# Performance work log

Measured on AMD Instinct MI355X. Metric: run time of the kernel, lower is better.

The kernel has to match this reference:

```python
import jax, jax.numpy as jnp
import numpy as np
from jax.scipy.special import logsumexp

T, N, C, L = 2048, 256, 128, 200
S = 2 * L + 1  # padded label length (blanks interleaved)
NEG = -1e30    # finite -inf surrogate (safe for logsumexp grads)


def setup_inputs() -> dict:
    key = jax.random.key(0)
    k1, k2 = jax.random.split(key)
    # module consumes pred as log-probabilities (adds scores in log space)
    pred = jax.nn.log_softmax(jax.random.normal(k1, (T, N, C), dtype=jnp.float32), axis=-1)
    target = jax.random.randint(k2, (N * L,), 1, C)  # labels in [1, C-1], 0 is blank
    input_length = jnp.full((N,), T, dtype=jnp.int32)
    target_length = jnp.full((N,), L, dtype=jnp.int32)
    return {"pred": pred, "target": target, "input_length": input_length, "target_length": target_length}


def _ctc_loss(pred, target, target_length):
    # Faithful to the original's slicing: start_i = target_length[i-1] for i>0 else 0
    starts = jnp.concatenate([jnp.zeros((1,), jnp.int32), target_length[:-1].astype(jnp.int32)])
    idx = starts[:, None] + jnp.arange(L)[None, :]                     # (N, L)
    labels = target[idx]                                               # (N, L)
    # padded target: blank(0) at even positions, labels at odd positions
    ext = jnp.zeros((N, S), dtype=target.dtype).at[:, 1::2].set(labels)
    pos = jnp.arange(S)
    prev2 = jnp.pad(ext, ((0, 0), (2, 0)))[:, :S]
    # skip transition s-2 -> s allowed iff s is a non-blank position and label differs from s-2
    skip_ok = (pos % 2 == 1)[None, :] & (pos >= 2)[None, :] & (ext != prev2)  # (N, S)

    emit0 = jnp.take_along_axis(pred[0], ext, axis=1)                  # (N, S)
    alpha0 = jnp.full((N, S), NEG, jnp.float32).at[:, 0].set(emit0[:, 0]).at[:, 1].set(emit0[:, 1])

    def step(alpha, pred_t):
        sc = jnp.take_along_axis(pred_t, ext, axis=1)                  # (N, S) emission log-probs
        a1 = jnp.concatenate([jnp.full((N, 1), NEG, alpha.dtype), alpha[:, :-1]], axis=1)
        a2 = jnp.concatenate([jnp.full((N, 2), NEG, alpha.dtype), alpha[:, :-2]], axis=1)
        a2 = jnp.where(skip_ok, a2, NEG)
        new = logsumexp(jnp.stack([alpha, a1, a2], axis=0), axis=0) + sc
        return new, None

    alphaT, _ = jax.lax.scan(step, alpha0, pred[1:])
    # per-sample loss: -logsumexp(alpha[T-1, S-2], alpha[T-1, S-1])
    loss = -logsumexp(alphaT[:, S - 2:], axis=1)                        # (N,)
    return jnp.sum(loss)  # reduction='sum'


def reference(pred, target, input_length, target_length):
    return _ctc_loss(pred, target, target_length)
```

## Files before the change

kernel.cpp:

```cpp
#include <hip/hip_runtime.h>


#define TT 2048
#define NN 256
#define CC 128
#define LL 200

#define K_LOG2E 1.4426950408889634f
#define K_LN2   0.6931471805599453f
#define NEGB   (-1.44e30f)
#define PEN    (-2.0e30f)
#define NC4    131072u

__device__ __forceinline__ float max3f(float a, float b, float c) {
    float r; asm("v_max3_f32 %0, %1, %2, %3" : "=v"(r) : "v"(a), "v"(b), "v"(c)); return r;
}

__global__ __launch_bounds__(256, 1)
void ctc_alpha(const float* __restrict__ pred,
               const int* __restrict__ target,
               const int* __restrict__ tlen,
               float* __restrict__ loss_ws)
{
    __shared__ float blk[5][128][16];
    __shared__ int   flags[8];

    const int tid  = threadIdx.x;
    const int wid  = tid >> 6;
    const int lane = tid & 63;
    const int n    = blockIdx.x;

    if (tid < 8) flags[tid] = (tid >= 4) ? 0x7fffffff : 0;
    for (int i = tid; i < 128 * 16; i += 256) ((float*)blk[4])[i] = PEN;

    const int start = (n == 0) ? 0 : tlen[n - 1];
    const int idx   = (wid << 6) | lane;
    int lab1 = 0; float msk1 = 0.0f;
    if (idx < LL) {
        lab1 = target[start + idx];
        if (idx >= 1 && lab1 != target[start + idx - 1]) msk1 = 1.0f;
    }

    float al0, al1;
    {
        const float eB = pred[n * CC];
        const float eL = pred[n * CC + lab1];
        al0 = (idx == 0) ? K_LOG2E * eB : NEGB;
        al1 = (idx == 0) ? K_LOG2E * eL : NEGB;
    }
    __syncthreads();

    const char* pcRow = (const char*)pred + (size_t)(NN * CC + n * CC) * 4u;
    uint32_t vB = 0u;
    uint32_t vL = (uint32_t)lab1 * 4u;
    asm volatile("" : "+v"(vB), "+v"(vL));
    float scB[16], scL[16];
#pragma unroll
    for (int ph = 0; ph < 16; ++ph) {
        scB[ph] = *(const float*)(pcRow + vB);
        scL[ph] = *(const float*)(pcRow + vL);
        pcRow += NC4;
    }

    float (* const blkC)[16] = blk[(wid == 0) ? 4 : (wid - 1)];
    float (* const blkW)[16] = blk[wid];
    volatile int* pflag = &flags[(wid == 0) ? 7 : (wid - 1)];
    volatile int* mflag = &flags[wid];
    int fval = *pflag;

    float bndA[16], bndB[16], bw[16];
    float bprev = (wid == 0) ? PEN : NEGB;

#define LOAD_BLK(DST, B)                                                       \
    {                                                                          \
        const float4* q = (const float4*)&blkC[B][0];                          \
        const float4 v0 = q[0], v1 = q[1], v2 = q[2], v3 = q[3];               \
        DST[0]=v0.x;  DST[1]=v0.y;  DST[2]=v0.z;  DST[3]=v0.w;                 \
        DST[4]=v1.x;  DST[5]=v1.y;  DST[6]=v1.z;  DST[7]=v1.w;                 \
        DST[8]=v2.x;  DST[9]=v2.y;  DST[10]=v2.z; DST[11]=v2.w;                \
        DST[12]=v3.x; DST[13]=v3.y; DST[14]=v3.z; DST[15]=v3.w;                \
    }

#define STORE_BLK(B)                                                           \
    if (lane == 63) {                                                          \
        float4* d = (float4*)&blkW[B][0];                                      \
        d[0] = make_float4(bw[0],  bw[1],  bw[2],  bw[3]);                     \
        d[1] = make_float4(bw[4],  bw[5],  bw[6],  bw[7]);                     \
        d[2] = make_float4(bw[8],  bw[9],  bw[10], bw[11]);                    \
        d[3] = make_float4(bw[12], bw[13], bw[14], bw[15]);                    \
    }

#define CTC_STEP(PH, BV, PREF)                                                 \
    {                                                                          \
        const float hold = ((PH) == 0) ? bprev : BV[((PH) + 15) & 15];         \
        const int h1i = __builtin_amdgcn_update_dpp(                           \
            __float_as_int(hold), __float_as_int(al1), 0x138, 0xf, 0xf, false);\
        const float h1 = __int_as_float(h1i);                                  \
        const float M  = max3f(al1, al0, h1);                                  \
        const float b1 = fmaf(K_LOG2E, scL[PH], M);                            \
        const float b0 = fmaf(K_LOG2E, scB[PH], M);                            \
        const float e1 = __builtin_amdgcn_exp2f(al1 - M);                      \
        const float e0 = __builtin_amdgcn_exp2f(al0 - M);                      \
        const float eh = __builtin_amdgcn_exp2f(h1 - M);                       \
        const float s1 = fmaf(eh, msk1, e1 + e0);                              \
        const float s0 = e0 + eh;                                              \
        al1 = b1 + __builtin_amdgcn_logf(s1);                                  \
        al0 = b0 + __builtin_amdgcn_logf(s0);                                  \
        bw[PH] = al1;                                                          \
        if (PREF) {                                                            \
            scB[PH] = *(const float*)(pcRow + vB);                             \
            scL[PH] = *(const float*)(pcRow + vL);                             \
            pcRow += NC4;                                                      \
        }                                                                      \
    }

#define RUN_BLOCK(B, BUSE, BPRE, NEED, LASTPREF)                               \
    {                                                                          \
        const int need_ = (NEED);                                              \
        if (fval < need_) { do { fval = *pflag; } while (fval < need_); }      \
        asm volatile("" ::: "memory");                                         \
        LOAD_BLK(BPRE, (B) + 1)                                                \
        CTC_STEP( 0, BUSE, 1) CTC_STEP( 1, BUSE, 1) CTC_STEP( 2, BUSE, 1)      \
        CTC_STEP( 3, BUSE, 1) CTC_STEP( 4, BUSE, 1) CTC_STEP( 5, BUSE, 1)      \
        CTC_STEP( 6, BUSE, 1) CTC_STEP( 7, BUSE, 1) CTC_STEP( 8, BUSE, 1)      \
        CTC_STEP( 9, BUSE, 1) CTC_STEP(10, BUSE, 1) CTC_STEP(11, BUSE, 1)      \
        CTC_STEP(12, BUSE, 1) CTC_STEP(13, BUSE, 1) CTC_STEP(14, BUSE, 1)      \
        CTC_STEP(15, BUSE, LASTPREF)                                           \
        STORE_BLK(B)                                                           \
        asm volatile("" ::: "memory");             \
        if (lane == 0) *mflag = (B) + 1;                                       \
        bprev = BUSE[15];                                                      \
        fval = *pflag;                                                         \
    }

    if (fval < 1) { do { fval = *pflag; } while (fval < 1); }
    asm volatile("" ::: "memory");
    LOAD_BLK(bndA, 0)

    for (int bb = 0; bb < 63; ++bb) {
        RUN_BLOCK(2 * bb,     bndA, bndB, 2 * bb + 2, 1)
        RUN_BLOCK(2 * bb + 1, bndB, bndA, 2 * bb + 3, 1)
    }

    RUN_BLOCK(126, bndA, bndB, 128, 0)

    {
        asm volatile("" ::: "memory");
        CTC_STEP( 0, bndB, 0) CTC_STEP( 1, bndB, 0) CTC_STEP( 2, bndB, 0)
        CTC_STEP( 3, bndB, 0) CTC_STEP( 4, bndB, 0) CTC_STEP( 5, bndB, 0)
        CTC_STEP( 6, bndB, 0) CTC_STEP( 7, bndB, 0) CTC_STEP( 8, bndB, 0)
        CTC_STEP( 9, bndB, 0) CTC_STEP(10, bndB, 0) CTC_STEP(11, bndB, 0)
        CTC_STEP(12, bndB, 0) CTC_STEP(13, bndB, 0) CTC_STEP(14, bndB, 0)
        STORE_BLK(127)
        asm volatile("" ::: "memory");
        if (lane == 0) *mflag = 128;
    }
#undef CTC_STEP
#undef RUN_BLOCK
#undef LOAD_BLK
#undef STORE_BLK

    const float A = __shfl(al1, 7, 64);
    const float B = __shfl(al0, 8, 64);
    if (wid == 3 && lane == 0) {
        const float m  = fmaxf(A, B);
        const float ls = m + __builtin_amdgcn_logf(
            __builtin_amdgcn_exp2f(A - m) + __builtin_amdgcn_exp2f(B - m));
        loss_ws[n] = -ls * K_LN2;
    }
}

__global__ void ctc_reduce(const float* __restrict__ ws, float* __restrict__ out)
{
    const int tid = threadIdx.x;
    float v = ws[tid];
    v += __shfl_down(v, 32);
    v += __shfl_down(v, 16);
    v += __shfl_down(v, 8);
    v += __shfl_down(v, 4);
    v += __shfl_down(v, 2);
    v += __shfl_down(v, 1);
    __shared__ float p[4];
    if ((tid & 63) == 0) p[tid >> 6] = v;
    __syncthreads();
    if (tid == 0) out[0] = (p[0] + p[1]) + (p[2] + p[3]);
}

extern "C" void kernel_launch(void* const* d_in, const int* in_sizes, int n_in,
                              void* d_out, int out_size, void* d_ws, size_t ws_size,
                              hipStream_t stream)
{
    const float* pred   = (const float*)d_in[0];
    const int*   target = (const int*)d_in[1];
    const int*   tlen   = (const int*)d_in[3];
    float* ws = (float*)d_ws;

    ctc_alpha<<<NN, 256, 0, stream>>>(pred, target, tlen, ws);
    ctc_reduce<<<1, NN, 0, stream>>>(ws, (float*)d_out);
}
```

Baseline: 151.0 us.

## Represent CTC alpha as mantissa-exponent pairs instead of log-space values

Replaces the log-space recurrence (max3, three exp2 and two log per step) with a scaled linear-domain form: each alpha is stored as a float mantissa plus an integer exponent. Terms are aligned with ldexp to the maximum exponent and multiplied by exp2 of the emission, and the values are renormalised every four steps. The aim is to drop the transcendental log on the serial dependency chain, but it doubles the DPP shuffles, doubles LDS boundary traffic and register use, and adds integer and ldexp work. It also relies on the mantissas not underflowing between renormalisations.

```diff
diff --git a/kernel.cpp b/kernel.cpp
--- a/kernel.cpp
+++ b/kernel.cpp
@@ -8,13 +8,8 @@
 
 #define K_LOG2E 1.4426950408889634f
 #define K_LN2   0.6931471805599453f
-#define NEGB   (-1.44e30f)
-#define PEN    (-2.0e30f)
-#define NC4    131072u
-
-__device__ __forceinline__ float max3f(float a, float b, float c) {
-    float r; asm("v_max3_f32 %0, %1, %2, %3" : "=v"(r) : "v"(a), "v"(b), "v"(c)); return r;
-}
+#define EDEAD   (-(1 << 28))
+#define NC4     131072u
 
 __global__ __launch_bounds__(256, 1)
 void ctc_alpha(const float* __restrict__ pred,
@@ -22,7 +17,8 @@
                const int* __restrict__ tlen,
                float* __restrict__ loss_ws)
 {
-    __shared__ float blk[5][128][16];
+    __shared__ float blkM[5][128][16];
+    __shared__ int   blkE[5][128][16];
     __shared__ int   flags[8];
 
     const int tid  = threadIdx.x;
@@ -31,7 +27,10 @@
     const int n    = blockIdx.x;
 
     if (tid < 8) flags[tid] = (tid >= 4) ? 0x7fffffff : 0;
-    for (int i = tid; i < 128 * 16; i += 256) ((float*)blk[4])[i] = PEN;
+    for (int i = tid; i < 128 * 16; i += 256) {
+        ((float*)blkM[4])[i] = 0.0f;
+        ((int*)blkE[4])[i]   = EDEAD;
+    }
 
     const int start = (n == 0) ? 0 : tlen[n - 1];
     const int idx   = (wid << 6) | lane;
@@ -41,12 +40,15 @@
         if (idx >= 1 && lab1 != target[start + idx - 1]) msk1 = 1.0f;
     }
 
-    float al0, al1;
+    float m0, m1; int E0, E1;
     {
-        const float eB = pred[n * CC];
-        const float eL = pred[n * CC + lab1];
-        al0 = (idx == 0) ? K_LOG2E * eB : NEGB;
-        al1 = (idx == 0) ? K_LOG2E * eL : NEGB;
+        const float xB = K_LOG2E * pred[n * CC];
+        const float xL = K_LOG2E * pred[n * CC + lab1];
+        const float fB = floorf(xB), fL = floorf(xL);
+        m0 = (idx == 0) ? __builtin_amdgcn_exp2f(xB - fB) : 0.0f;
+        m1 = (idx == 0) ? __builtin_amdgcn_exp2f(xL - fL) : 0.0f;
+        E0 = (idx == 0) ? (int)fB : EDEAD;
+        E1 = (idx == 0) ? (int)fL : EDEAD;
     }
     __syncthreads();
 
@@ -62,51 +64,75 @@
         pcRow += NC4;
     }
 
-    float (* const blkC)[16] = blk[(wid == 0) ? 4 : (wid - 1)];
-    float (* const blkW)[16] = blk[wid];
+    float (* const blkCM)[16] = blkM[(wid == 0) ? 4 : (wid - 1)];
+    int   (* const blkCE)[16] = blkE[(wid == 0) ? 4 : (wid - 1)];
+    float (* const blkWM)[16] = blkM[wid];
+    int   (* const blkWE)[16] = blkE[wid];
     volatile int* pflag = &flags[(wid == 0) ? 7 : (wid - 1)];
     volatile int* mflag = &flags[wid];
     int fval = *pflag;
 
-    float bndA[16], bndB[16], bw[16];
-    float bprev = (wid == 0) ? PEN : NEGB;
-
-#define LOAD_BLK(DST, B)                                                       \
+    float bndAM[16], bndBM[16], bwM[16];
+    int   bndAE[16], bndBE[16], bwE[16];
+    float bprevM = 0.0f;
+    int   bprevE = EDEAD;
+
+#define LOAD_BLK(DM, DE, B)                                                    \
     {                                                                          \
-        const float4* q = (const float4*)&blkC[B][0];                          \
-        const float4 v0 = q[0], v1 = q[1], v2 = q[2], v3 = q[3];               \
-        DST[0]=v0.x;  DST[1]=v0.y;  DST[2]=v0.z;  DST[3]=v0.w;                 \
-        DST[4]=v1.x;  DST[5]=v1.y;  DST[6]=v1.z;  DST[7]=v1.w;                 \
-        DST[8]=v2.x;  DST[9]=v2.y;  DST[10]=v2.z; DST[11]=v2.w;                \
-        DST[12]=v3.x; DST[13]=v3.y; DST[14]=v3.z; DST[15]=v3.w;                \
+        const float4* qm = (const float4*)&blkCM[B][0];                        \
+        const int4*   qe = (const int4*)&blkCE[B][0];                          \
+        const float4 a0 = qm[0], a1 = qm[1], a2 = qm[2], a3 = qm[3];           \
+        const int4   b0 = qe[0], b1 = qe[1], b2 = qe[2], b3 = qe[3];           \
+        DM[0]=a0.x;  DM[1]=a0.y;  DM[2]=a0.z;  DM[3]=a0.w;                     \
+        DM[4]=a1.x;  DM[5]=a1.y;  DM[6]=a1.z;  DM[7]=a1.w;                     \
+        DM[8]=a2.x;  DM[9]=a2.y;  DM[10]=a2.z; DM[11]=a2.w;                    \
+        DM[12]=a3.x; DM[13]=a3.y; DM[14]=a3.z; DM[15]=a3.w;                    \
+        DE[0]=b0.x;  DE[1]=b0.y;  DE[2]=b0.z;  DE[3]=b0.w;                     \
+        DE[4]=b1.x;  DE[5]=b1.y;  DE[6]=b1.z;  DE[7]=b1.w;                     \
+        DE[8]=b2.x;  DE[9]=b2.y;  DE[10]=b2.z; DE[11]=b2.w;                    \
+        DE[12]=b3.x; DE[13]=b3.y; DE[14]=b3.z; DE[15]=b3.w;                    \
     }
 
 #define STORE_BLK(B)                                                           \
     if (lane == 63) {                                                          \
-        float4* d = (float4*)&blkW[B][0];                                      \
-        d[0] = make_float4(bw[0],  bw[1],  bw[2],  bw[3]);                     \
-        d[1] = make_float4(bw[4],  bw[5],  bw[6],  bw[7]);                     \
-        d[2] = make_float4(bw[8],  bw[9],  bw[10], bw[11]);                    \
-        d[3] = make_float4(bw[12], bw[13], bw[14], bw[15]);                    \
-    }
-
-#define CTC_STEP(PH, BV, PREF)                                                 \
+        float4* dm = (float4*)&blkWM[B][0];                                    \
+        int4*   de = (int4*)&blkWE[B][0];                                      \
+        dm[0] = make_float4(bwM[0],  bwM[1],  bwM[2],  bwM[3]);                \
+        dm[1] = make_float4(bwM[4],  bwM[5],  bwM[6],  bwM[7]);                \
+        dm[2] = make_float4(bwM[8],  bwM[9],  bwM[10], bwM[11]);               \
+        dm[3] = make_float4(bwM[12], bwM[13], bwM[14], bwM[15]);               \
+        de[0] = make_int4(bwE[0],  bwE[1],  bwE[2],  bwE[3]);                  \
+        de[1] = make_int4(bwE[4],  bwE[5],  bwE[6],  bwE[7]);                  \
+        de[2] = make_int4(bwE[8],  bwE[9],  bwE[10], bwE[11]);                 \
+        de[3] = make_int4(bwE[12], bwE[13], bwE[14], bwE[15]);                 \
+    }
+
+#define CTC_STEP(PH, BVM, BVE, PREF)                                           \
     {                                                                          \
-        const float hold = ((PH) == 0) ? bprev : BV[((PH) + 15) & 15];         \
-        const int h1i = __builtin_amdgcn_update_dpp(                           \
-            __float_as_int(hold), __float_as_int(al1), 0x138, 0xf, 0xf, false);\
-        const float h1 = __int_as_float(h1i);                                  \
-        const float M  = max3f(al1, al0, h1);                                  \
-        const float b1 = fmaf(K_LOG2E, scL[PH], M);                            \
-        const float b0 = fmaf(K_LOG2E, scB[PH], M);                            \
-        const float e1 = __builtin_amdgcn_exp2f(al1 - M);                      \
-        const float e0 = __builtin_amdgcn_exp2f(al0 - M);                      \
-        const float eh = __builtin_amdgcn_exp2f(h1 - M);                       \
-        const float s1 = fmaf(eh, msk1, e1 + e0);                              \
-        const float s0 = e0 + eh;                                              \
-        al1 = b1 + __builtin_amdgcn_logf(s1);                                  \
-        al0 = b0 + __builtin_amdgcn_logf(s0);                                  \
-        bw[PH] = al1;                                                          \
+        const float holdM = ((PH) == 0) ? bprevM : BVM[((PH) + 15) & 15];      \
+        const int   holdE = ((PH) == 0) ? bprevE : BVE[((PH) + 15) & 15];      \
+        const int mhi = __builtin_amdgcn_update_dpp(                           \
+            __float_as_int(holdM), __float_as_int(m1), 0x138, 0xf, 0xf, false);\
+        const int Eh  = __builtin_amdgcn_update_dpp(                           \
+            holdE, E1, 0x138, 0xf, 0xf, false);                                \
+        const float mh = __int_as_float(mhi);                                  \
+        const int Emax = max(max(E1, E0), Eh);                                 \
+        const float t1 = ldexpf(m1, E1 - Emax);                                \
+        const float t0 = ldexpf(m0, E0 - Emax);                                \
+        const float th = ldexpf(mh, Eh - Emax);                                \
+        const float eL = __builtin_amdgcn_exp2f(K_LOG2E * scL[PH]);            \
+        const float eB = __builtin_amdgcn_exp2f(K_LOG2E * scB[PH]);            \
+        const float s1 = (t1 + t0) + th * msk1;                                \
+        const float s0 = t0 + th;                                              \
+        m1 = s1 * eL;  E1 = Emax;                                              \
+        m0 = s0 * eB;  E0 = Emax;                                              \
+        bwM[PH] = m1;  bwE[PH] = E1;                                           \
+        if (((PH) & 3) == 3) {       \
+            const int e1 = (int)((__float_as_uint(m1) >> 23) & 255u) - 126;    \
+            m1 = ldexpf(m1, -e1);  E1 += e1;                                   \
+            const int e0 = (int)((__float_as_uint(m0) >> 23) & 255u) - 126;    \
+            m0 = ldexpf(m0, -e0);  E0 += e0;                                   \
+        }                                                                      \
         if (PREF) {                                                            \
             scB[PH] = *(const float*)(pcRow + vB);                             \
             scL[PH] = *(const float*)(pcRow + vL);                             \
@@ -114,43 +140,46 @@
         }                                                                      \
     }
 
-#define RUN_BLOCK(B, BUSE, BPRE, NEED, LASTPREF)                               \
+#define RUN_BLOCK(B, UM, UE, PM, PE, NEED, LASTPREF)                           \
     {                                                                          \
         const int need_ = (NEED);                                              \
         if (fval < need_) { do { fval = *pflag; } while (fval < need_); }      \
         asm volatile("" ::: "memory");                                         \
-        LOAD_BLK(BPRE, (B) + 1)                                                \
-        CTC_STEP( 0, BUSE, 1) CTC_STEP( 1, BUSE, 1) CTC_STEP( 2, BUSE, 1)      \
-        CTC_STEP( 3, BUSE, 1) CTC_STEP( 4, BUSE, 1) CTC_STEP( 5, BUSE, 1)      \
-        CTC_STEP( 6, BUSE, 1) CTC_STEP( 7, BUSE, 1) CTC_STEP( 8, BUSE, 1)      \
-        CTC_STEP( 9, BUSE, 1) CTC_STEP(10, BUSE, 1) CTC_STEP(11, BUSE, 1)      \
-        CTC_STEP(12, BUSE, 1) CTC_STEP(13, BUSE, 1) CTC_STEP(14, BUSE, 1)      \
-        CTC_STEP(15, BUSE, LASTPREF)                                           \
+        LOAD_BLK(PM, PE, (B) + 1)                                              \
+        CTC_STEP( 0, UM, UE, 1) CTC_STEP( 1, UM, UE, 1) CTC_STEP( 2, UM, UE, 1)\
+        CTC_STEP( 3, UM, UE, 1) CTC_STEP( 4, UM, UE, 1) CTC_STEP( 5, UM, UE, 1)\
+        CTC_STEP( 6, UM, UE, 1) CTC_STEP( 7, UM, UE, 1) CTC_STEP( 8, UM, UE, 1)\
+        CTC_STEP( 9, UM, UE, 1) CTC_STEP(10, UM, UE, 1) CTC_STEP(11, UM, UE, 1)\
+        CTC_STEP(12, UM, UE, 1) CTC_STEP(13, UM, UE, 1) CTC_STEP(14, UM, UE, 1)\
+        CTC_STEP(15, UM, UE, LASTPREF)                                         \
         STORE_BLK(B)                                                           \
         asm volatile("" ::: "memory");             \
         if (lane == 0) *mflag = (B) + 1;                                       \
-        bprev = BUSE[15];                                                      \
+        bprevM = UM[15];  bprevE = UE[15];                                     \
         fval = *pflag;                                                         \
     }
 
     if (fval < 1) { do { fval = *pflag; } while (fval < 1); }
     asm volatile("" ::: "memory");
-    LOAD_BLK(bndA, 0)
+    LOAD_BLK(bndAM, bndAE, 0)
 
     for (int bb = 0; bb < 63; ++bb) {
-        RUN_BLOCK(2 * bb,     bndA, bndB, 2 * bb + 2, 1)
-        RUN_BLOCK(2 * bb + 1, bndB, bndA, 2 * bb + 3, 1)
-    }
-
-    RUN_BLOCK(126, bndA, bndB, 128, 0)
+        RUN_BLOCK(2 * bb,     bndAM, bndAE, bndBM, bndBE, 2 * bb + 2, 1)
+        RUN_BLOCK(2 * bb + 1, bndBM, bndBE, bndAM, bndAE, 2 * bb + 3, 1)
+    }
+
+    RUN_BLOCK(126, bndAM, bndAE, bndBM, bndBE, 128, 0)
 
     {
         asm volatile("" ::: "memory");
-        CTC_STEP( 0, bndB, 0) CTC_STEP( 1, bndB, 0) CTC_STEP( 2, bndB, 0)
-        CTC_STEP( 3, bndB, 0) CTC_STEP( 4, bndB, 0) CTC_STEP( 5, bndB, 0)
-        CTC_STEP( 6, bndB, 0) CTC_STEP( 7, bndB, 0) CTC_STEP( 8, bndB, 0)
-        CTC_STEP( 9, bndB, 0) CTC_STEP(10, bndB, 0) CTC_STEP(11, bndB, 0)
-        CTC_STEP(12, bndB, 0) CTC_STEP(13, bndB, 0) CTC_STEP(14, bndB, 0)
+        CTC_STEP( 0, bndBM, bndBE, 0) CTC_STEP( 1, bndBM, bndBE, 0)
+        CTC_STEP( 2, bndBM, bndBE, 0) CTC_STEP( 3, bndBM, bndBE, 0)
+        CTC_STEP( 4, bndBM, bndBE, 0) CTC_STEP( 5, bndBM, bndBE, 0)
+        CTC_STEP( 6, bndBM, bndBE, 0) CTC_STEP( 7, bndBM, bndBE, 0)
+        CTC_STEP( 8, bndBM, bndBE, 0) CTC_STEP( 9, bndBM, bndBE, 0)
+        CTC_STEP(10, bndBM, bndBE, 0) CTC_STEP(11, bndBM, bndBE, 0)
+        CTC_STEP(12, bndBM, bndBE, 0) CTC_STEP(13, bndBM, bndBE, 0)
+        CTC_STEP(14, bndBM, bndBE, 0)
         STORE_BLK(127)
         asm volatile("" ::: "memory");
         if (lane == 0) *mflag = 128;
@@ -160,10 +189,14 @@
 #undef LOAD_BLK
 #undef STORE_BLK
 
-    const float A = __shfl(al1, 7, 64);
-    const float B = __shfl(al0, 8, 64);
+    const float Am = __shfl(m1, 7, 64);
+    const int   Ae = __shfl(E1, 7, 64);
+    const float Bm = __shfl(m0, 8, 64);
+    const int   Be = __shfl(E0, 8, 64);
     if (wid == 3 && lane == 0) {
-        const float m  = fmaxf(A, B);
+        const float A = (float)Ae + __builtin_amdgcn_logf(Am);
+        const float B = (float)Be + __builtin_amdgcn_logf(Bm);
+        const float m = fmaxf(A, B);
         const float ls = m + __builtin_amdgcn_logf(
             __builtin_amdgcn_exp2f(A - m) + __builtin_amdgcn_exp2f(B - m));
         loss_ws[n] = -ls * K_LN2;
```

New measurement: 159.9 us. 1.06x slower.

## Stream emission rows into an LDS ring via global_load_lds instead of per-lane gathers

Applied to the files above, without the earlier changes.

Replaces the per-lane register prefetch of blank and label emissions, 16 timesteps deep, with a per-wave LDS ring buffer. Each wave copies whole 128-class pred rows into the ring with coalesced global_load_lds, then reads the blank and label scores from LDS a few steps ahead. Hand-counted s_waitcnt vmcnt values enforce ordering. The aim is to cut scattered global gathers and register pressure, at the cost of extra LDS traffic and fragile manual wait counts.

```diff
diff --git a/kernel.cpp b/kernel.cpp
--- a/kernel.cpp
+++ b/kernel.cpp
@@ -10,7 +10,10 @@
 #define K_LN2   0.6931471805599453f
 #define NEGB   (-1.44e30f)
 #define PEN    (-2.0e30f)
-#define NC4    131072u
+#define NCW    (NN * CC)
+
+typedef const void __attribute__((address_space(1)))* gas_ptr;
+typedef void __attribute__((address_space(3)))* las_ptr;
 
 __device__ __forceinline__ float max3f(float a, float b, float c) {
     float r; asm("v_max3_f32 %0, %1, %2, %3" : "=v"(r) : "v"(a), "v"(b), "v"(c)); return r;
@@ -23,6 +26,7 @@
                float* __restrict__ loss_ws)
 {
     __shared__ float blk[5][128][16];
+    __shared__ float ring[4][16][CC];
     __shared__ int   flags[8];
 
     const int tid  = threadIdx.x;
@@ -50,17 +54,26 @@
     }
     __syncthreads();
 
-    const char* pcRow = (const char*)pred + (size_t)(NN * CC + n * CC) * 4u;
-    uint32_t vB = 0u;
-    uint32_t vL = (uint32_t)lab1 * 4u;
-    asm volatile("" : "+v"(vB), "+v"(vL));
-    float scB[16], scL[16];
+    asm volatile("s_waitcnt vmcnt(0)" ::: "memory");
+
+    {
+        const float* src = pred + NCW + n * CC + lane;
 #pragma unroll
-    for (int ph = 0; ph < 16; ++ph) {
-        scB[ph] = *(const float*)(pcRow + vB);
-        scL[ph] = *(const float*)(pcRow + vL);
-        pcRow += NC4;
-    }
+        for (int j = 1; j <= 16; ++j) {
+            __builtin_amdgcn_global_load_lds((gas_ptr)src,
+                                             (las_ptr)&ring[wid][j & 15][0],  4, 0, 0);
+            __builtin_amdgcn_global_load_lds((gas_ptr)(src + 64),
+                                             (las_ptr)&ring[wid][j & 15][64], 4, 0, 0);
+            src += NCW;
+        }
+    }
+    const float* gp  = pred + (size_t)17 * NCW + n * CC + lane;
+    const float* gp2 = gp + 64;
+
+    float sB[4], sL[4];
+    asm volatile("s_waitcnt vmcnt(28)" ::: "memory");
+    sB[1] = ring[wid][1][0];  sL[1] = ring[wid][1][lab1];
+    sB[2] = ring[wid][2][0];  sL[2] = ring[wid][2][lab1];
 
     float (* const blkC)[16] = blk[(wid == 0) ? 4 : (wid - 1)];
     float (* const blkW)[16] = blk[wid];
@@ -90,15 +103,27 @@
         d[3] = make_float4(bw[12], bw[13], bw[14], bw[15]);                    \
     }
 
-#define CTC_STEP(PH, BV, PREF)                                                 \
+#define CTC_STEP(PH, BV, VM, PREF, GATHER)                                     \
     {                                                                          \
+        if (PREF) {                                                            \
+            __builtin_amdgcn_global_load_lds((gas_ptr)gp,                      \
+                (las_ptr)&ring[wid][(1 + (PH)) & 15][0],  4, 0, 0);            \
+            __builtin_amdgcn_global_load_lds((gas_ptr)gp2,                     \
+                (las_ptr)&ring[wid][(1 + (PH)) & 15][64], 4, 0, 0);            \
+            gp += NCW; gp2 += NCW;                                             \
+        }                                                                      \
+        asm volatile("s_waitcnt vmcnt(%0)" :: "i"(VM) : "memory");             \
+        if (GATHER) {                                                          \
+            sB[(3 + (PH)) & 3] = ring[wid][(3 + (PH)) & 15][0];                \
+            sL[(3 + (PH)) & 3] = ring[wid][(3 + (PH)) & 15][lab1];             \
+        }                                                                      \
         const float hold = ((PH) == 0) ? bprev : BV[((PH) + 15) & 15];         \
         const int h1i = __builtin_amdgcn_update_dpp(                           \
             __float_as_int(hold), __float_as_int(al1), 0x138, 0xf, 0xf, false);\
         const float h1 = __int_as_float(h1i);                                  \
         const float M  = max3f(al1, al0, h1);                                  \
-        const float b1 = fmaf(K_LOG2E, scL[PH], M);                            \
-        const float b0 = fmaf(K_LOG2E, scB[PH], M);                            \
+        const float b1 = fmaf(K_LOG2E, sL[(1 + (PH)) & 3], M);                 \
+        const float b0 = fmaf(K_LOG2E, sB[(1 + (PH)) & 3], M);                 \
         const float e1 = __builtin_amdgcn_exp2f(al1 - M);                      \
         const float e0 = __builtin_amdgcn_exp2f(al0 - M);                      \
         const float eh = __builtin_amdgcn_exp2f(h1 - M);                       \
@@ -107,25 +132,22 @@
         al1 = b1 + __builtin_amdgcn_logf(s1);                                  \
         al0 = b0 + __builtin_amdgcn_logf(s0);                                  \
         bw[PH] = al1;                                                          \
-        if (PREF) {                                                            \
-            scB[PH] = *(const float*)(pcRow + vB);                             \
-            scL[PH] = *(const float*)(pcRow + vL);                             \
-            pcRow += NC4;                                                      \
-        }                                                                      \
-    }
-
-#define RUN_BLOCK(B, BUSE, BPRE, NEED, LASTPREF)                               \
+    }
+
+#define RUN_BLOCK(B, BUSE, BPRE, NEED, LASTPREF, LASTVM)                       \
     {                                                                          \
         const int need_ = (NEED);                                              \
         if (fval < need_) { do { fval = *pflag; } while (fval < need_); }      \
         asm volatile("" ::: "memory");                                         \
         LOAD_BLK(BPRE, (B) + 1)                                                \
-        CTC_STEP( 0, BUSE, 1) CTC_STEP( 1, BUSE, 1) CTC_STEP( 2, BUSE, 1)      \
-        CTC_STEP( 3, BUSE, 1) CTC_STEP( 4, BUSE, 1) CTC_STEP( 5, BUSE, 1)      \
-        CTC_STEP( 6, BUSE, 1) CTC_STEP( 7, BUSE, 1) CTC_STEP( 8, BUSE, 1)      \
-        CTC_STEP( 9, BUSE, 1) CTC_STEP(10, BUSE, 1) CTC_STEP(11, BUSE, 1)      \
-        CTC_STEP(12, BUSE, 1) CTC_STEP(13, BUSE, 1) CTC_STEP(14, BUSE, 1)      \
-        CTC_STEP(15, BUSE, LASTPREF)                                           \
+        CTC_STEP( 0, BUSE, 28, 1, 1) CTC_STEP( 1, BUSE, 28, 1, 1)              \
+        CTC_STEP( 2, BUSE, 28, 1, 1) CTC_STEP( 3, BUSE, 28, 1, 1)              \
+        CTC_STEP( 4, BUSE, 28, 1, 1) CTC_STEP( 5, BUSE, 28, 1, 1)              \
+        CTC_STEP( 6, BUSE, 28, 1, 1) CTC_STEP( 7, BUSE, 28, 1, 1)              \
+        CTC_STEP( 8, BUSE, 28, 1, 1) CTC_STEP( 9, BUSE, 28, 1, 1)              \
+        CTC_STEP(10, BUSE, 28, 1, 1) CTC_STEP(11, BUSE, 28, 1, 1)              \
+        CTC_STEP(12, BUSE, 28, 1, 1) CTC_STEP(13, BUSE, 28, 1, 1)              \
+        CTC_STEP(14, BUSE, 28, 1, 1) CTC_STEP(15, BUSE, LASTVM, LASTPREF, 1)   \
         STORE_BLK(B)                                                           \
         asm volatile("" ::: "memory");             \
         if (lane == 0) *mflag = (B) + 1;                                       \
@@ -138,19 +160,22 @@
     LOAD_BLK(bndA, 0)
 
     for (int bb = 0; bb < 63; ++bb) {
-        RUN_BLOCK(2 * bb,     bndA, bndB, 2 * bb + 2, 1)
-        RUN_BLOCK(2 * bb + 1, bndB, bndA, 2 * bb + 3, 1)
-    }
-
-    RUN_BLOCK(126, bndA, bndB, 128, 0)
+        RUN_BLOCK(2 * bb,     bndA, bndB, 2 * bb + 2, 1, 28)
+        RUN_BLOCK(2 * bb + 1, bndB, bndA, 2 * bb + 3, 1, 28)
+    }
+
+    RUN_BLOCK(126, bndA, bndB, 128, 0, 26)
 
     {
         asm volatile("" ::: "memory");
-        CTC_STEP( 0, bndB, 0) CTC_STEP( 1, bndB, 0) CTC_STEP( 2, bndB, 0)
-        CTC_STEP( 3, bndB, 0) CTC_STEP( 4, bndB, 0) CTC_STEP( 5, bndB, 0)
-        CTC_STEP( 6, bndB, 0) CTC_STEP( 7, bndB, 0) CTC_STEP( 8, bndB, 0)
-        CTC_STEP( 9, bndB, 0) CTC_STEP(10, bndB, 0) CTC_STEP(11, bndB, 0)
-        CTC_STEP(12, bndB, 0) CTC_STEP(13, bndB, 0) CTC_STEP(14, bndB, 0)
+        CTC_STEP( 0, bndB, 24, 0, 1) CTC_STEP( 1, bndB, 22, 0, 1)
+        CTC_STEP( 2, bndB, 20, 0, 1) CTC_STEP( 3, bndB, 18, 0, 1)
+        CTC_STEP( 4, bndB, 16, 0, 1) CTC_STEP( 5, bndB, 14, 0, 1)
+        CTC_STEP( 6, bndB, 12, 0, 1) CTC_STEP( 7, bndB, 10, 0, 1)
+        CTC_STEP( 8, bndB,  8, 0, 1) CTC_STEP( 9, bndB,  6, 0, 1)
+        CTC_STEP(10, bndB,  4, 0, 1) CTC_STEP(11, bndB,  2, 0, 1)
+        CTC_STEP(12, bndB,  0, 0, 1) CTC_STEP(13, bndB,  0, 0, 0)
+        CTC_STEP(14, bndB,  0, 0, 0)
         STORE_BLK(127)
         asm volatile("" ::: "memory");
         if (lane == 0) *mflag = 128;
```

Measured after the change: 574.2 us. +280.3%, slower.

## Double-buffer emission prefetch with inline-asm loads and explicit vmcnt waits

Applied to the files above, without the earlier changes.

Replaces the per-step rolling emission prefetch with two 16-step register buffers. A whole block of 32 global loads is issued in inline asm one block ahead, and a single s_waitcnt vmcnt(32) waits only for the previous block's data before computing. This is meant to take the compiler's conservative waitcnt placement and load scheduling out of the serial recurrence's critical path. In exchange it costs more VGPRs, and the hand-placed waitcnt and sched_barrier must stay correct.

```diff
diff --git a/kernel.cpp b/kernel.cpp
--- a/kernel.cpp
+++ b/kernel.cpp
@@ -50,17 +50,49 @@
     }
     __syncthreads();
 
-    const char* pcRow = (const char*)pred + (size_t)(NN * CC + n * CC) * 4u;
+    const char* rp = (const char*)pred + (size_t)(NN * CC + n * CC) * 4u;
     uint32_t vB = 0u;
     uint32_t vL = (uint32_t)lab1 * 4u;
     asm volatile("" : "+v"(vB), "+v"(vL));
-    float scB[16], scL[16];
-#pragma unroll
-    for (int ph = 0; ph < 16; ++ph) {
-        scB[ph] = *(const float*)(pcRow + vB);
-        scL[ph] = *(const float*)(pcRow + vL);
-        pcRow += NC4;
-    }
+
+    float sAB[16], sAL[16], sBB[16], sBL[16];
+
+#define PREF_SC(PB, PL)                                                        \
+    {                                                                          \
+        _Pragma("unroll")                                                      \
+        for (int j = 0; j < 16; ++j) {                                         \
+            asm volatile("global_load_dword %0, %1, %2"                        \
+                : "=&v"(PB[j]) : "v"(vB), "s"(rp) : "memory");                 \
+            asm volatile("global_load_dword %0, %1, %2"                        \
+                : "=&v"(PL[j]) : "v"(vL), "s"(rp) : "memory");                 \
+            rp += NC4;                                                         \
+        }                                                                      \
+    }
+#define PREF_SC_CLAMP(PB, PL)                                                  \
+    {                                                                          \
+        _Pragma("unroll")                                                      \
+        for (int j = 0; j < 15; ++j) {                                         \
+            asm volatile("global_load_dword %0, %1, %2"                        \
+                : "=&v"(PB[j]) : "v"(vB), "s"(rp) : "memory");                 \
+            asm volatile("global_load_dword %0, %1, %2"                        \
+                : "=&v"(PL[j]) : "v"(vL), "s"(rp) : "memory");                 \
+            rp += NC4;                                                         \
+        }                                                                      \
+        const char* rp2 = rp - NC4;                                            \
+        asm volatile("global_load_dword %0, %1, %2"                            \
+            : "=&v"(PB[15]) : "v"(vB), "s"(rp2) : "memory");                   \
+        asm volatile("global_load_dword %0, %1, %2"                            \
+            : "=&v"(PL[15]) : "v"(vL), "s"(rp2) : "memory");                   \
+    }
+
+#define KA(S)                                                                  \
+    asm volatile("" : "+v"(S[0]), "+v"(S[1]), "+v"(S[2]),  "+v"(S[3]),         \
+                      "+v"(S[4]), "+v"(S[5]), "+v"(S[6]),  "+v"(S[7]));        \
+    asm volatile("" : "+v"(S[8]), "+v"(S[9]), "+v"(S[10]), "+v"(S[11]),        \
+                      "+v"(S[12]),"+v"(S[13]),"+v"(S[14]), "+v"(S[15]));
+
+    asm volatile("s_waitcnt vmcnt(0)" ::: "memory");
+    PREF_SC(sAB, sAL)
 
     float (* const blkC)[16] = blk[(wid == 0) ? 4 : (wid - 1)];
     float (* const blkW)[16] = blk[wid];
@@ -90,15 +122,15 @@
         d[3] = make_float4(bw[12], bw[13], bw[14], bw[15]);                    \
     }
 
-#define CTC_STEP(PH, BV, PREF)                                                 \
+#define CTC_STEP(PH, BV, UB, UL)                                               \
     {                                                                          \
         const float hold = ((PH) == 0) ? bprev : BV[((PH) + 15) & 15];         \
         const int h1i = __builtin_amdgcn_update_dpp(                           \
             __float_as_int(hold), __float_as_int(al1), 0x138, 0xf, 0xf, false);\
         const float h1 = __int_as_float(h1i);                                  \
         const float M  = max3f(al1, al0, h1);                                  \
-        const float b1 = fmaf(K_LOG2E, scL[PH], M);                            \
-        const float b0 = fmaf(K_LOG2E, scB[PH], M);                            \
+        const float b1 = fmaf(K_LOG2E, UL[PH], M);                             \
+        const float b0 = fmaf(K_LOG2E, UB[PH], M);                             \
         const float e1 = __builtin_amdgcn_exp2f(al1 - M);                      \
         const float e0 = __builtin_amdgcn_exp2f(al0 - M);                      \
         const float eh = __builtin_amdgcn_exp2f(h1 - M);                       \
@@ -107,25 +139,26 @@
         al1 = b1 + __builtin_amdgcn_logf(s1);                                  \
         al0 = b0 + __builtin_amdgcn_logf(s0);                                  \
         bw[PH] = al1;                                                          \
-        if (PREF) {                                                            \
-            scB[PH] = *(const float*)(pcRow + vB);                             \
-            scL[PH] = *(const float*)(pcRow + vL);                             \
-            pcRow += NC4;                                                      \
-        }                                                                      \
-    }
-
-#define RUN_BLOCK(B, BUSE, BPRE, NEED, LASTPREF)                               \
-    {                                                                          \
+    }
+
+#define RUN_BLOCK(B, UB, UL, PB, PL, BUSE, BPRE, NEED, CLAMP)                  \
+    {                                                                          \
+        if (CLAMP) { PREF_SC_CLAMP(PB, PL) } else { PREF_SC(PB, PL) }          \
         const int need_ = (NEED);                                              \
         if (fval < need_) { do { fval = *pflag; } while (fval < need_); }      \
         asm volatile("" ::: "memory");                                         \
         LOAD_BLK(BPRE, (B) + 1)                                                \
-        CTC_STEP( 0, BUSE, 1) CTC_STEP( 1, BUSE, 1) CTC_STEP( 2, BUSE, 1)      \
-        CTC_STEP( 3, BUSE, 1) CTC_STEP( 4, BUSE, 1) CTC_STEP( 5, BUSE, 1)      \
-        CTC_STEP( 6, BUSE, 1) CTC_STEP( 7, BUSE, 1) CTC_STEP( 8, BUSE, 1)      \
-        CTC_STEP( 9, BUSE, 1) CTC_STEP(10, BUSE, 1) CTC_STEP(11, BUSE, 1)      \
-        CTC_STEP(12, BUSE, 1) CTC_STEP(13, BUSE, 1) CTC_STEP(14, BUSE, 1)      \
-        CTC_STEP(15, BUSE, LASTPREF)                                           \
+        asm volatile("s_waitcnt vmcnt(32)" ::: "memory");    \
+        __builtin_amdgcn_sched_barrier(0);                                     \
+        KA(UB) KA(UL)                             \
+        CTC_STEP( 0, BUSE, UB, UL) CTC_STEP( 1, BUSE, UB, UL)                  \
+        CTC_STEP( 2, BUSE, UB, UL) CTC_STEP( 3, BUSE, UB, UL)                  \
+        CTC_STEP( 4, BUSE, UB, UL) CTC_STEP( 5, BUSE, UB, UL)                  \
+        CTC_STEP( 6, BUSE, UB, UL) CTC_STEP( 7, BUSE, UB, UL)                  \
+        CTC_STEP( 8, BUSE, UB, UL) CTC_STEP( 9, BUSE, UB, UL)                  \
+        CTC_STEP(10, BUSE, UB, UL) CTC_STEP(11, BUSE, UB, UL)                  \
+        CTC_STEP(12, BUSE, UB, UL) CTC_STEP(13, BUSE, UB, UL)                  \
+        CTC_STEP(14, BUSE, UB, UL) CTC_STEP(15, BUSE, UB, UL)                  \
         STORE_BLK(B)                                                           \
         asm volatile("" ::: "memory");             \
         if (lane == 0) *mflag = (B) + 1;                                       \
@@ -138,19 +171,24 @@
     LOAD_BLK(bndA, 0)
 
     for (int bb = 0; bb < 63; ++bb) {
-        RUN_BLOCK(2 * bb,     bndA, bndB, 2 * bb + 2, 1)
-        RUN_BLOCK(2 * bb + 1, bndB, bndA, 2 * bb + 3, 1)
-    }
-
-    RUN_BLOCK(126, bndA, bndB, 128, 0)
+        RUN_BLOCK(2 * bb,     sAB, sAL, sBB, sBL, bndA, bndB, 2 * bb + 2, 0)
+        RUN_BLOCK(2 * bb + 1, sBB, sBL, sAB, sAL, bndB, bndA, 2 * bb + 3, 0)
+    }
+
+    RUN_BLOCK(126, sAB, sAL, sBB, sBL, bndA, bndB, 128, 1)
 
     {
-        asm volatile("" ::: "memory");
-        CTC_STEP( 0, bndB, 0) CTC_STEP( 1, bndB, 0) CTC_STEP( 2, bndB, 0)
-        CTC_STEP( 3, bndB, 0) CTC_STEP( 4, bndB, 0) CTC_STEP( 5, bndB, 0)
-        CTC_STEP( 6, bndB, 0) CTC_STEP( 7, bndB, 0) CTC_STEP( 8, bndB, 0)
-        CTC_STEP( 9, bndB, 0) CTC_STEP(10, bndB, 0) CTC_STEP(11, bndB, 0)
-        CTC_STEP(12, bndB, 0) CTC_STEP(13, bndB, 0) CTC_STEP(14, bndB, 0)
+        asm volatile("s_waitcnt vmcnt(0)" ::: "memory");
+        __builtin_amdgcn_sched_barrier(0);
+        KA(sBB) KA(sBL)
+        CTC_STEP( 0, bndB, sBB, sBL) CTC_STEP( 1, bndB, sBB, sBL)
+        CTC_STEP( 2, bndB, sBB, sBL) CTC_STEP( 3, bndB, sBB, sBL)
+        CTC_STEP( 4, bndB, sBB, sBL) CTC_STEP( 5, bndB, sBB, sBL)
+        CTC_STEP( 6, bndB, sBB, sBL) CTC_STEP( 7, bndB, sBB, sBL)
+        CTC_STEP( 8, bndB, sBB, sBL) CTC_STEP( 9, bndB, sBB, sBL)
+        CTC_STEP(10, bndB, sBB, sBL) CTC_STEP(11, bndB, sBB, sBL)
+        CTC_STEP(12, bndB, sBB, sBL) CTC_STEP(13, bndB, sBB, sBL)
+        CTC_STEP(14, bndB, sBB, sBL)
         STORE_BLK(127)
         asm volatile("" ::: "memory");
         if (lane == 0) *mflag = 128;
@@ -159,6 +197,9 @@
 #undef RUN_BLOCK
 #undef LOAD_BLK
 #undef STORE_BLK
+#undef PREF_SC
+#undef PREF_SC_CLAMP
+#undef KA
 
     const float A = __shfl(al1, 7, 64);
     const float B = __shfl(al0, 8, 64);
```

After: 143.2 us, median of 2. 5.2% less time.
